# Kernel tuning notes

Measured on AMD Instinct MI355X. Metric: run time of the kernel, lower is better.

Reference implementation:

```python
import jax, jax.numpy as jnp
import numpy as np

HEADS = 12
D_MODEL = 768
D_K = D_MODEL // HEADS


def setup_inputs() -> dict:
    key = jax.random.key(0)
    ks = jax.random.split(key, 11)
    B, S, D = 2, 2048, D_MODEL
    s = 1.0 / np.sqrt(D)
    return {
        "query": jax.random.normal(ks[0], (B, S, D), jnp.float32),
        "key": jax.random.normal(ks[1], (B, S, D), jnp.float32),
        "value": jax.random.normal(ks[2], (B, S, D), jnp.float32),
        "Wq": jax.random.normal(ks[3], (D, D), jnp.float32) * s,
        "bq": jnp.zeros((D,), jnp.float32),
        "Wk": jax.random.normal(ks[4], (D, D), jnp.float32) * s,
        "bk": jnp.zeros((D,), jnp.float32),
        "Wv": jax.random.normal(ks[5], (D, D), jnp.float32) * s,
        "bv": jnp.zeros((D,), jnp.float32),
        "Wo": jax.random.normal(ks[6], (D, D), jnp.float32) * s,
        "bo": jnp.zeros((D,), jnp.float32),
    }


def reference(query, key, value, Wq, bq, Wk, bk, Wv, bv, Wo, bo):
    B, S, D = query.shape
    # linear projections (weights stored as [in, out])
    q = query @ Wq + bq
    k = key @ Wk + bk
    v = value @ Wv + bv
    # [B, H, S, d_k]
    q = q.reshape(B, S, HEADS, D_K).transpose(0, 2, 1, 3)
    k = k.reshape(B, S, HEADS, D_K).transpose(0, 2, 1, 3)
    v = v.reshape(B, S, HEADS, D_K).transpose(0, 2, 1, 3)
    # scores: note module scales by sqrt(d_k) (key.size(-1)), not self.scaled
    scores = jnp.einsum("bhqd,bhkd->bhqk", q, k) / jnp.sqrt(jnp.asarray(D_K, q.dtype))
    weights = jax.nn.softmax(scores, axis=-1)
    context = jnp.einsum("bhqk,bhkd->bhqd", weights, v)
    context = context.transpose(0, 2, 1, 3).reshape(B, S, D)
    return context @ Wo + bo
```

## Files before the change

### kernel.cpp

```cpp
#include <hip/hip_runtime.h>
#include <hip/hip_bf16.h>
#include <math.h>

#define D_MODEL 768
#define HEADS 12
#define DK 64
#define SEQ 2048
#define BATCH 2
#define MTOT (BATCH * SEQ)
#define QSCALE 0.18033688011112042f

using short8 = __attribute__((ext_vector_type(8))) short;
using us4    = __attribute__((ext_vector_type(4))) unsigned short;
using f32x4  = __attribute__((ext_vector_type(4))) float;

static __device__ __forceinline__ unsigned f2bf2(float x, float y) {
    __hip_bfloat162 t = __float22bfloat162_rn(float2{x, y});
    return *reinterpret_cast<unsigned*>(&t);
}
static __device__ __forceinline__ unsigned short f2bf1(float x) {
    __hip_bfloat16 t = __float2bfloat16(x);
    return *reinterpret_cast<unsigned short*>(&t);
}
static __device__ __forceinline__ float bf2f(unsigned short u) {
    unsigned v = (unsigned)u << 16;
    return __uint_as_float(v);
}
static __device__ __forceinline__ short8 cvt8(float4 a, float4 b) {
    union { unsigned u[4]; short8 s; } r;
    r.u[0] = f2bf2(a.x, a.y);
    r.u[1] = f2bf2(a.z, a.w);
    r.u[2] = f2bf2(b.x, b.y);
    r.u[3] = f2bf2(b.z, b.w);
    return r.s;
}
static __device__ __forceinline__ float fast_exp2(float x) {
#if __has_builtin(__builtin_amdgcn_exp2f)
    return __builtin_amdgcn_exp2f(x);
#else
    return __expf(x * 0.6931471805599453f);
#endif
}

static __device__ __forceinline__ void gload_lds16(const void* g, void* l) {
    __builtin_amdgcn_global_load_lds(
        (const __attribute__((address_space(1))) void*)g,
        (__attribute__((address_space(3))) void*)l, 16, 0, 0);
}

static __device__ __forceinline__ void barrier_lgkm() {
    asm volatile("s_waitcnt lgkmcnt(0)" ::: "memory");
    __builtin_amdgcn_s_barrier();
    __builtin_amdgcn_sched_barrier(0);
}
static __device__ __forceinline__ void barrier_vm0() {
    asm volatile("s_waitcnt vmcnt(0)" ::: "memory");
    __builtin_amdgcn_s_barrier();
    __builtin_amdgcn_sched_barrier(0);
}

__global__ __launch_bounds__(256) void cvt_wt_k(
    const float* __restrict__ Wq, const float* __restrict__ Wk,
    const float* __restrict__ Wv, const float* __restrict__ Wo,
    unsigned short* __restrict__ Wqt, unsigned short* __restrict__ Wkt,
    unsigned short* __restrict__ Wvt, unsigned short* __restrict__ Wot)
{
    const int z = blockIdx.z;
    const float* W = z == 0 ? Wq : z == 1 ? Wk : z == 2 ? Wv : Wo;
    unsigned short* Wt = z == 0 ? Wqt : z == 1 ? Wkt : z == 2 ? Wvt : Wot;
    __shared__ float t[32][33];
    const int n0 = blockIdx.x * 32, k0 = blockIdx.y * 32;
    const int tx = threadIdx.x & 31;
    const int ty0 = (threadIdx.x >> 5) * 4;
    #pragma unroll
    for (int j = 0; j < 4; ++j)
        t[ty0 + j][tx] = W[(size_t)(k0 + ty0 + j) * D_MODEL + n0 + tx];
    __syncthreads();
    #pragma unroll
    for (int j = 0; j < 4; ++j)
        Wt[(size_t)(n0 + ty0 + j) * D_MODEL + k0 + tx] = f2bf1(t[tx][ty0 + j]);
}

__global__ __launch_bounds__(512) void gemm_qkv_k(
    const float* __restrict__ query, const float* __restrict__ key,
    const float* __restrict__ value,
    const unsigned short* __restrict__ Wqt, const unsigned short* __restrict__ Wkt,
    const unsigned short* __restrict__ Wvt,
    const float* __restrict__ bq, const float* __restrict__ bk,
    const float* __restrict__ bv,
    unsigned short* __restrict__ qb, unsigned short* __restrict__ kb,
    unsigned short* __restrict__ vb)
{
    __shared__ __align__(16) char gsm[65536];

    const int bid = blockIdx.x;
    const int xcd = bid & 7;
    const int idx = bid >> 3;
    const int z   = idx / 24;
    const int rr  = idx % 24;
    const int brow = (xcd * 4 + rr / 6) * 128;
    const int bcol = (rr % 6) * 128;

    const float* A           = z == 0 ? query : z == 1 ? key : value;
    const unsigned short* Wt = z == 0 ? Wqt : z == 1 ? Wkt : Wvt;
    const float* bias        = z == 0 ? bq  : z == 1 ? bk  : bv;
    unsigned short* C        = z == 0 ? qb  : z == 1 ? kb  : vb;
    const float scale        = z == 0 ? QSCALE : 1.0f;

    const int tid  = threadIdx.x;
    const int w    = tid >> 6;
    const int lane = tid & 63;
    const int g    = lane >> 4, c = lane & 15;
    const int wr   = w >> 2, wc = w & 3;

    f32x4 acc[4][2] = {};

    const int xc  = (c & 7) << 4;
    const int rb0 = c * 128 + ((g * 16) ^ xc);
    const int rb1 = c * 128 + ((64 + g * 16) ^ xc);

    int bsrow[2], bsoff[2], bsdst[2];
    #pragma unroll
    for (int r = 0; r < 2; ++r) {
        int phys = (w * 2 + r) * 1024 + lane * 16;
        int row  = phys >> 7;
        int slot = (phys >> 4) & 7;
        bsrow[r] = row;
        bsoff[r] = (slot ^ (row & 7)) * 8;
        bsdst[r] = (w * 2 + r) * 1024;
    }
    const int ar = tid >> 2;
    const int ac = (tid & 3) << 4;
    int awa[2];
    #pragma unroll
    for (int i = 0; i < 2; ++i)
        awa[i] = ar * 128 + (((ac << 1) + 16 * i) ^ ((ar & 7) << 4));
    const float* Ap32 = A + (size_t)(brow + ar) * D_MODEL + ac;

    float4 ra0, ra1, ra2, ra3;

    auto stageB = [&](int k0, int buf) {
        #pragma unroll
        for (int r = 0; r < 2; ++r)
            gload_lds16(Wt + (size_t)(bcol + bsrow[r]) * D_MODEL + k0 + bsoff[r],
                        gsm + 32768 + buf * 16384 + bsdst[r]);
    };
    auto loadA32 = [&](int k0) {
        ra0 = *(const float4*)(Ap32 + k0);
        ra1 = *(const float4*)(Ap32 + k0 + 4);
        ra2 = *(const float4*)(Ap32 + k0 + 8);
        ra3 = *(const float4*)(Ap32 + k0 + 12);
    };
    auto writeA32 = [&](int buf) {
        *(short8*)(gsm + buf * 16384 + awa[0]) = cvt8(ra0, ra1);
        *(short8*)(gsm + buf * 16384 + awa[1]) = cvt8(ra2, ra3);
    };

    stageB(0, 0);
    loadA32(0);
    writeA32(0);
    barrier_lgkm();

    for (int k0 = 0; k0 < D_MODEL; k0 += 128) {
        #pragma unroll
        for (int u = 0; u < 2; ++u) {
            const int kn = min(k0 + u * 64 + 64, D_MODEL - 64);
            stageB(kn, u ^ 1);
            loadA32(kn);
            __builtin_amdgcn_sched_barrier(0);

            __builtin_amdgcn_s_setprio(1);
            #pragma unroll
            for (int kstep = 0; kstep < 2; ++kstep) {
                const int rb = kstep ? rb1 : rb0;
                short8 af[4], bf[2];
                #pragma unroll
                for (int m = 0; m < 4; ++m)
                    af[m] = *(const short8*)(gsm + u * 16384 + wr * 8192 +
                                             m * 2048 + rb);
                #pragma unroll
                for (int n = 0; n < 2; ++n)
                    bf[n] = *(const short8*)(gsm + 32768 + u * 16384 +
                                             wc * 4096 + n * 2048 + rb);
                #pragma unroll
                for (int m = 0; m < 4; ++m)
                    #pragma unroll
                    for (int n = 0; n < 2; ++n)
                        acc[m][n] = __builtin_amdgcn_mfma_f32_16x16x32_bf16(
                                        af[m], bf[n], acc[m][n], 0, 0, 0);
            }
            __builtin_amdgcn_s_setprio(0);

            writeA32(u ^ 1);
            barrier_lgkm();
        }
    }

    #pragma unroll
    for (int m = 0; m < 4; ++m)
        #pragma unroll
        for (int n = 0; n < 2; ++n) {
            const int col = bcol + wc * 32 + n * 16 + c;
            const float bval = bias[col];
            #pragma unroll
            for (int j = 0; j < 4; ++j) {
                const int row = brow + wr * 64 + m * 16 + g * 4 + j;
                C[(size_t)row * D_MODEL + col] = f2bf1((acc[m][n][j] + bval) * scale);
            }
        }
}

__global__ __launch_bounds__(256) void gemm_o_k(
    const unsigned short* __restrict__ A, const unsigned short* __restrict__ Wt,
    const float* __restrict__ bias, float* __restrict__ C)
{
    __shared__ __align__(16) char gsm[32768];

    const int bid = blockIdx.x;
    const int xcd = bid & 7;
    const int idx = bid >> 3;
    const int brow = (xcd * 8 + idx / 12) * 64;
    const int bcol = (idx % 12) * 64;

    const int tid  = threadIdx.x;
    const int w    = tid >> 6;
    const int lane = tid & 63;
    const int g    = lane >> 4, c = lane & 15;
    const int wr   = w >> 1, wc = w & 1;

    f32x4 acc[2][2] = {{f32x4{0,0,0,0}, f32x4{0,0,0,0}},
                       {f32x4{0,0,0,0}, f32x4{0,0,0,0}}};

    const int xc  = (c & 7) << 4;
    const int rb0 = c * 128 + ((g * 16) ^ xc);
    const int rb1 = c * 128 + ((64 + g * 16) ^ xc);
    const int a0 = rb0 + wr * 4096, a1 = rb1 + wr * 4096;
    const int b0r = rb0 + 16384 + wc * 4096, b1r = rb1 + 16384 + wc * 4096;

    int bsrow[2], bsoff[2], bsdst[2];
    #pragma unroll
    for (int r = 0; r < 2; ++r) {
        int phys = (w + 4 * r) * 1024 + lane * 16;
        int row  = phys >> 7;
        int slot = (phys >> 4) & 7;
        bsrow[r] = row;
        bsoff[r] = (slot ^ (row & 7)) * 8;
        bsdst[r] = (w + 4 * r) * 1024;
    }

    auto stage = [&](int k0, int buf) {
        #pragma unroll
        for (int r = 0; r < 2; ++r) {
            gload_lds16(A  + (size_t)(brow + bsrow[r]) * D_MODEL + k0 + bsoff[r],
                        gsm + buf * 8192 + bsdst[r]);
            gload_lds16(Wt + (size_t)(bcol + bsrow[r]) * D_MODEL + k0 + bsoff[r],
                        gsm + 16384 + buf * 8192 + bsdst[r]);
        }
    };

    stage(0, 0);
    barrier_vm0();

    for (int k0 = 0; k0 < D_MODEL; k0 += 128) {
        #pragma unroll
        for (int u = 0; u < 2; ++u) {
            const int kn = min(k0 + u * 64 + 64, D_MODEL - 64);
            stage(kn, u ^ 1);
            __builtin_amdgcn_sched_barrier(0);

            #pragma unroll
            for (int kstep = 0; kstep < 2; ++kstep) {
                short8 af[2], bf[2];
                #pragma unroll
                for (int m = 0; m < 2; ++m)
                    af[m] = *(const short8*)(gsm + u * 8192 + m * 2048 +
                                             (kstep ? a1 : a0));
                #pragma unroll
                for (int n = 0; n < 2; ++n)
                    bf[n] = *(const short8*)(gsm + u * 8192 + n * 2048 +
                                             (kstep ? b1r : b0r));
                #pragma unroll
                for (int m = 0; m < 2; ++m)
                    #pragma unroll
                    for (int n = 0; n < 2; ++n)
                        acc[m][n] = __builtin_amdgcn_mfma_f32_16x16x32_bf16(
                                        af[m], bf[n], acc[m][n], 0, 0, 0);
            }
            barrier_vm0();
        }
    }

    #pragma unroll
    for (int m = 0; m < 2; ++m)
        #pragma unroll
        for (int n = 0; n < 2; ++n) {
            const int col = bcol + wc * 32 + n * 16 + c;
            const float bval = bias[col];
            #pragma unroll
            for (int j = 0; j < 4; ++j) {
                const int row = brow + wr * 32 + m * 16 + g * 4 + j;
                C[(size_t)row * D_MODEL + col] = acc[m][n][j] + bval;
            }
        }
}

__global__ __launch_bounds__(512) void attn_mfma_k(
    const unsigned short* __restrict__ q, const unsigned short* __restrict__ k,
    const unsigned short* __restrict__ v, unsigned short* __restrict__ opart,
    float* __restrict__ mlpart)
{
    __shared__ __align__(16) char sm[49152];

    const int tid  = threadIdx.x;
    const int w    = tid >> 6;
    const int lane = tid & 63;
    const int g    = lane >> 4;
    const int c    = lane & 15;

    const int bid  = blockIdx.x;
    const int swz  = (bid & 7) * 96 + (bid >> 3);
    const int qt   = swz & 15;
    const int rest = swz >> 4;
    const int half = rest & 1;
    const int hb   = rest >> 1;
    const int h    = hb % HEADS;
    const int b    = hb / HEADS;
    const int q0   = qt * 128;
    const int NT2  = 16;

    short8 qf0, qf1;
    {
        const int qrow = q0 + (w << 4) + c;
        const unsigned short* qp = q + (size_t)(b * SEQ + qrow) * D_MODEL + h * DK;
        qf0 = *(const short8*)(qp + g * 8);
        qf1 = *(const short8*)(qp + 32 + g * 8);
    }

    float m_run[4] = {-INFINITY, -INFINITY, -INFINITY, -INFINITY};
    f32x4 lacc = f32x4{0, 0, 0, 0};
    f32x4 o[4] = {f32x4{0,0,0,0}, f32x4{0,0,0,0}, f32x4{0,0,0,0}, f32x4{0,0,0,0}};
    const short8 ONES = {0x3F80, 0x3F80, 0x3F80, 0x3F80,
                         0x3F80, 0x3F80, 0x3F80, 0x3F80};

    const int xc  = (c & 7) << 4;
    const int rb0 = c * 128 + ((g * 16) ^ xc);
    const int rb1 = c * 128 + ((64 + g * 16) ^ xc);
    const int bp0 = 32768 + w * 2048 + rb0;
    const int bp1 = 32768 + w * 2048 + rb1;

    int pwa[4];
    #pragma unroll
    for (int r = 0; r < 4; ++r) {
        const int row = (g << 2) + r;
        pwa[r] = 32768 + w * 2048 + row * 128 + ((c << 3) ^ ((row & 7) << 4));
    }
    const int cv = tid & 15, vd0 = ((tid >> 4) & 15) << 2;
    int vwa[4];
    #pragma unroll
    for (int j = 0; j < 4; ++j) {
        const int row = vd0 + j;
        vwa[j] = 16384 + row * 128 + ((cv << 3) ^ ((row & 7) << 4));
    }
    int kdst[2];
    const unsigned short* kg[2];
    {
        const unsigned short* kbase =
            k + (size_t)(b * SEQ + half * (SEQ / 2)) * D_MODEL + h * DK;
        #pragma unroll
        for (int r = 0; r < 2; ++r) {
            int phys = ((w & 3) + 4 * r) * 1024 + lane * 16;
            int row  = phys >> 7;
            int slot = (phys >> 4) & 7;
            kdst[r]  = ((w & 3) + 4 * r) * 1024;
            kg[r]    = kbase + (size_t)row * D_MODEL + (slot ^ (row & 7)) * 8;
        }
    }
    const unsigned short* vg =
        v + (size_t)(b * SEQ + half * (SEQ / 2) + cv) * D_MODEL + h * DK + vd0;
    const int TS = 64 * D_MODEL;

    us4 va, vb_, vc, vd;

    if (w < 4) {
        gload_lds16(kg[0], sm + kdst[0]);
        gload_lds16(kg[1], sm + kdst[1]);
        va  = *(const us4*)(vg);
        vb_ = *(const us4*)(vg + 16 * D_MODEL);
        vc  = *(const us4*)(vg + 32 * D_MODEL);
        vd  = *(const us4*)(vg + 48 * D_MODEL);
        #pragma unroll
        for (int j = 0; j < 4; ++j) {
            uint2 pk;
            pk.x = (unsigned)va[j] | ((unsigned)vb_[j] << 16);
            pk.y = (unsigned)vc[j] | ((unsigned)vd[j] << 16);
            *(uint2*)(sm + vwa[j]) = pk;
        }
    }
    kg[0] += TS; kg[1] += TS; vg += TS;
    barrier_lgkm();

    for (int kt = 0; kt < NT2; kt += 2) {
        #pragma unroll
        for (int u = 0; u < 2; ++u) {
            if (w < 4) {
                gload_lds16(kg[0], sm + (u ^ 1) * 8192 + kdst[0]);
                gload_lds16(kg[1], sm + (u ^ 1) * 8192 + kdst[1]);
                va  = *(const us4*)(vg);
                vb_ = *(const us4*)(vg + 16 * D_MODEL);
                vc  = *(const us4*)(vg + 32 * D_MODEL);
                vd  = *(const us4*)(vg + 48 * D_MODEL);
            }
            kg[0] += TS; kg[1] += TS; vg += TS;
            __builtin_amdgcn_sched_barrier(0);

            f32x4 sacc[4] = {f32x4{0,0,0,0}, f32x4{0,0,0,0},
                             f32x4{0,0,0,0}, f32x4{0,0,0,0}};
            __builtin_amdgcn_s_setprio(1);
            #pragma unroll
            for (int kstep = 0; kstep < 2; ++kstep) {
                short8 af = kstep ? qf1 : qf0;
                #pragma unroll
                for (int ks = 0; ks < 4; ++ks) {
                    short8 bf = *(const short8*)(sm + u * 8192 + ks * 2048 +
                                                 (kstep ? rb1 : rb0));
                    sacc[ks] = __builtin_amdgcn_mfma_f32_16x16x32_bf16(
                                   af, bf, sacc[ks], 0, 0, 0);
                }
            }
            __builtin_amdgcn_s_setprio(0);

            float rm[4], dm;
            #pragma unroll
            for (int reg = 0; reg < 4; ++reg)
                rm[reg] = fmaxf(fmaxf(sacc[0][reg], sacc[1][reg]),
                                fmaxf(sacc[2][reg], sacc[3][reg]));
            dm = fmaxf(fmaxf(rm[0] - m_run[0], rm[1] - m_run[1]),
                       fmaxf(rm[2] - m_run[2], rm[3] - m_run[3]));
            if (__any(dm > 11.0f)) {
                #pragma unroll
                for (int reg = 0; reg < 4; ++reg) {
                    float mx = rm[reg];
                    mx = fmaxf(mx, __shfl_xor(mx, 1));
                    mx = fmaxf(mx, __shfl_xor(mx, 2));
                    mx = fmaxf(mx, __shfl_xor(mx, 4));
                    mx = fmaxf(mx, __shfl_xor(mx, 8));
                    const float mnew = fmaxf(m_run[reg], mx);
                    const float sc = fast_exp2(m_run[reg] - mnew);
                    m_run[reg] = mnew;
                    lacc[reg] *= sc;
                    o[0][reg] *= sc;
                    o[1][reg] *= sc;
                    o[2][reg] *= sc;
                    o[3][reg] *= sc;
                }
            }
            #pragma unroll
            for (int reg = 0; reg < 4; ++reg) {
                const float m = m_run[reg];
                float p0 = fast_exp2(sacc[0][reg] - m);
                float p1 = fast_exp2(sacc[1][reg] - m);
                float p2 = fast_exp2(sacc[2][reg] - m);
                float p3 = fast_exp2(sacc[3][reg] - m);
                uint2 pw;
                pw.x = f2bf2(p0, p1);
                pw.y = f2bf2(p2, p3);
                *(uint2*)(sm + pwa[reg]) = pw;
            }

            __builtin_amdgcn_s_setprio(1);
            #pragma unroll
            for (int kstep = 0; kstep < 2; ++kstep) {
                short8 paf = *(const short8*)(sm + (kstep ? bp1 : bp0));
                lacc = __builtin_amdgcn_mfma_f32_16x16x32_bf16(paf, ONES, lacc, 0, 0, 0);
                #pragma unroll
                for (int dsub = 0; dsub < 4; ++dsub) {
                    short8 vbf = *(const short8*)(sm + 16384 + u * 8192 +
                                                  dsub * 2048 + (kstep ? rb1 : rb0));
                    o[dsub] = __builtin_amdgcn_mfma_f32_16x16x32_bf16(
                                  paf, vbf, o[dsub], 0, 0, 0);
                }
            }
            __builtin_amdgcn_s_setprio(0);

            if (w < 4) {
                #pragma unroll
                for (int j = 0; j < 4; ++j) {
                    uint2 pk;
                    pk.x = (unsigned)va[j] | ((unsigned)vb_[j] << 16);
                    pk.y = (unsigned)vc[j] | ((unsigned)vd[j] << 16);
                    *(uint2*)(sm + (u ^ 1) * 8192 + vwa[j]) = pk;
                }
            }
            barrier_lgkm();
        }
    }

    const size_t obase = (size_t)half * ((size_t)MTOT * D_MODEL) +
                         (size_t)(b * SEQ) * D_MODEL + h * DK;
    #pragma unroll
    for (int reg = 0; reg < 4; ++reg) {
        const int qrow = q0 + (w << 4) + (g << 2) + reg;
        unsigned short* ob = opart + obase + (size_t)qrow * D_MODEL;
        #pragma unroll
        for (int dsub = 0; dsub < 4; ++dsub)
            ob[dsub * 16 + c] = f2bf1(o[dsub][reg]);
        if (c == 0) {
            float2 mlv;
            mlv.x = m_run[reg];
            mlv.y = lacc[reg];
            ((float2*)mlpart)[(size_t)half * MTOT * HEADS +
                              (size_t)(b * SEQ + qrow) * HEADS + h] = mlv;
        }
    }
}

__global__ __launch_bounds__(256) void combine_k(
    const unsigned short* __restrict__ op, const float* __restrict__ mlpart,
    unsigned short* __restrict__ cb)
{
    const int t   = blockIdx.x * 256 + threadIdx.x;
    const int row = t / 96;
    const int gi  = t - row * 96;
    const int col = gi << 3;
    const int h   = gi >> 3;

    const float2* mlp = (const float2*)mlpart;
    const float2 ml0 = mlp[(size_t)row * HEADS + h];
    const float2 ml1 = mlp[(size_t)MTOT * HEADS + (size_t)row * HEADS + h];
    const float m  = fmaxf(ml0.x, ml1.x);
    const float s0 = fast_exp2(ml0.x - m);
    const float s1 = fast_exp2(ml1.x - m);
    const float inv = 1.0f / (ml0.y * s0 + ml1.y * s1);
    const float a0 = s0 * inv, a1 = s1 * inv;

    const size_t off = (size_t)row * D_MODEL + col;
    us4 x0  = *(const us4*)(op + off);
    us4 x0b = *(const us4*)(op + off + 4);
    us4 x1  = *(const us4*)(op + (size_t)MTOT * D_MODEL + off);
    us4 x1b = *(const us4*)(op + (size_t)MTOT * D_MODEL + off + 4);

    union { unsigned short u[8]; short8 s; } r;
    #pragma unroll
    for (int j = 0; j < 4; ++j) {
        r.u[j]     = f2bf1(bf2f(x0[j])  * a0 + bf2f(x1[j])  * a1);
        r.u[4 + j] = f2bf1(bf2f(x0b[j]) * a0 + bf2f(x1b[j]) * a1);
    }
    *(short8*)(cb + off) = r.s;
}

extern "C" void kernel_launch(void* const* d_in, const int* in_sizes, int n_in,
                              void* d_out, int out_size, void* d_ws, size_t ws_size,
                              hipStream_t stream) {
    const float* query = (const float*)d_in[0];
    const float* key   = (const float*)d_in[1];
    const float* value = (const float*)d_in[2];
    const float* Wq = (const float*)d_in[3];
    const float* bq = (const float*)d_in[4];
    const float* Wk = (const float*)d_in[5];
    const float* bk = (const float*)d_in[6];
    const float* Wv = (const float*)d_in[7];
    const float* bv = (const float*)d_in[8];
    const float* Wo = (const float*)d_in[9];
    const float* bo = (const float*)d_in[10];
    float* out = (float*)d_out;

    const size_t mat = (size_t)MTOT * D_MODEL;
    unsigned short* qb  = (unsigned short*)d_ws;
    unsigned short* kb  = qb + mat;
    unsigned short* vb  = kb + mat;
    unsigned short* cb  = vb + mat;
    unsigned short* Wqt = cb + mat;
    unsigned short* Wkt = Wqt + (size_t)D_MODEL * D_MODEL;
    unsigned short* Wvt = Wkt + (size_t)D_MODEL * D_MODEL;
    unsigned short* Wot = Wvt + (size_t)D_MODEL * D_MODEL;
    unsigned short* op  = Wot + (size_t)D_MODEL * D_MODEL;
    float*          mlp = (float*)(op + 2 * mat);

    cvt_wt_k<<<dim3(D_MODEL / 32, D_MODEL / 32, 4), 256, 0, stream>>>(
        Wq, Wk, Wv, Wo, Wqt, Wkt, Wvt, Wot);

    gemm_qkv_k<<<dim3(576), 512, 0, stream>>>(
        query, key, value, Wqt, Wkt, Wvt, bq, bk, bv, qb, kb, vb);

    attn_mfma_k<<<dim3(768), 512, 0, stream>>>(qb, kb, vb, op, mlp);

    combine_k<<<dim3(MTOT * D_MODEL / 8 / 256), 256, 0, stream>>>(op, mlp, cb);

    gemm_o_k<<<dim3(768), 256, 0, stream>>>(cb, Wot, bo, out);
}
```

Baseline: 113.4 us.

## Rewrite attention with 32x32 MFMA, register-resident P, and 4-wave blocks

The attention kernel moves from 16x16x32 to 32x32x16 bf16 MFMA. It computes S^T so that the exponentiated probabilities stay in registers and feed the PV MFMA directly, with no round trip through LDS. Blocks shrink to 4 waves of 32 query rows each, with every wave loading K/V, and LDS drops to 32KB. The V LDS layout is permuted to match the new operand layout, and m/l are split into separate arrays. This removes the P store/load and barrier traffic and may raise occupancy, at the cost of a larger accumulator register footprint and a more complex layout mapping.

```diff
diff --git a/kernel.cpp b/kernel.cpp
--- a/kernel.cpp
+++ b/kernel.cpp
@@ -13,6 +13,7 @@
 using short8 = __attribute__((ext_vector_type(8))) short;
 using us4    = __attribute__((ext_vector_type(4))) unsigned short;
 using f32x4  = __attribute__((ext_vector_type(4))) float;
+using f32x16 = __attribute__((ext_vector_type(16))) float;
 
 static __device__ __forceinline__ unsigned f2bf2(float x, float y) {
     __hip_bfloat162 t = __float22bfloat162_rn(float2{x, y});
@@ -40,6 +41,11 @@
 #else
     return __expf(x * 0.6931471805599453f);
 #endif
+}
+static __device__ __forceinline__ unsigned pk2(float lo, float hi) {
+    unsigned d;
+    asm("v_cvt_pk_bf16_f32 %0, %1, %2" : "=v"(d) : "v"(lo), "v"(hi));
+    return d;
 }
 
 static __device__ __forceinline__ void gload_lds16(const void* g, void* l) {
@@ -304,18 +310,18 @@
         }
 }
 
-__global__ __launch_bounds__(512) void attn_mfma_k(
+__global__ __launch_bounds__(256) void attn_mfma_k(
     const unsigned short* __restrict__ q, const unsigned short* __restrict__ k,
     const unsigned short* __restrict__ v, unsigned short* __restrict__ opart,
-    float* __restrict__ mlpart)
+    float* __restrict__ mpart, float* __restrict__ lpart)
 {
-    __shared__ __align__(16) char sm[49152];
+    __shared__ __align__(16) char sm[32768];
 
     const int tid  = threadIdx.x;
     const int w    = tid >> 6;
     const int lane = tid & 63;
-    const int g    = lane >> 4;
-    const int c    = lane & 15;
+    const int c    = lane & 31;
+    const int hi   = lane >> 5;
 
     const int bid  = blockIdx.x;
     const int swz  = (bid & 7) * 96 + (bid >> 3);
@@ -328,39 +334,27 @@
     const int q0   = qt * 128;
     const int NT2  = 16;
 
-    short8 qf0, qf1;
+    short8 qf[4];
     {
-        const int qrow = q0 + (w << 4) + c;
-        const unsigned short* qp = q + (size_t)(b * SEQ + qrow) * D_MODEL + h * DK;
-        qf0 = *(const short8*)(qp + g * 8);
-        qf1 = *(const short8*)(qp + 32 + g * 8);
-    }
-
-    float m_run[4] = {-INFINITY, -INFINITY, -INFINITY, -INFINITY};
-    f32x4 lacc = f32x4{0, 0, 0, 0};
-    f32x4 o[4] = {f32x4{0,0,0,0}, f32x4{0,0,0,0}, f32x4{0,0,0,0}, f32x4{0,0,0,0}};
+        const unsigned short* qp =
+            q + (size_t)(b * SEQ + q0 + w * 32 + c) * D_MODEL + h * DK;
+        #pragma unroll
+        for (int t = 0; t < 4; ++t)
+            qf[t] = *(const short8*)(qp + t * 16 + hi * 8);
+    }
+
+    float m_run = -INFINITY;
+    f32x16 lacc = {};
+    f32x16 o0 = {}, o1 = {};
     const short8 ONES = {0x3F80, 0x3F80, 0x3F80, 0x3F80,
                          0x3F80, 0x3F80, 0x3F80, 0x3F80};
 
-    const int xc  = (c & 7) << 4;
-    const int rb0 = c * 128 + ((g * 16) ^ xc);
-    const int rb1 = c * 128 + ((64 + g * 16) ^ xc);
-    const int bp0 = 32768 + w * 2048 + rb0;
-    const int bp1 = 32768 + w * 2048 + rb1;
-
-    int pwa[4];
-    #pragma unroll
-    for (int r = 0; r < 4; ++r) {
-        const int row = (g << 2) + r;
-        pwa[r] = 32768 + w * 2048 + row * 128 + ((c << 3) ^ ((row & 7) << 4));
-    }
-    const int cv = tid & 15, vd0 = ((tid >> 4) & 15) << 2;
-    int vwa[4];
-    #pragma unroll
-    for (int j = 0; j < 4; ++j) {
-        const int row = vd0 + j;
-        vwa[j] = 16384 + row * 128 + ((cv << 3) ^ ((row & 7) << 4));
-    }
+    const int xc = (c & 7) << 4;
+    int koff[4];
+    #pragma unroll
+    for (int t = 0; t < 4; ++t)
+        koff[t] = ((32 * t + 16 * hi) ^ xc) + c * 128;
+
     int kdst[2];
     const unsigned short* kg[2];
     {
@@ -368,12 +362,20 @@
             k + (size_t)(b * SEQ + half * (SEQ / 2)) * D_MODEL + h * DK;
         #pragma unroll
         for (int r = 0; r < 2; ++r) {
-            int phys = ((w & 3) + 4 * r) * 1024 + lane * 16;
+            int phys = (w + 4 * r) * 1024 + lane * 16;
             int row  = phys >> 7;
             int slot = (phys >> 4) & 7;
-            kdst[r]  = ((w & 3) + 4 * r) * 1024;
+            kdst[r]  = (w + 4 * r) * 1024;
             kg[r]    = kbase + (size_t)row * D_MODEL + (slot ^ (row & 7)) * 8;
         }
+    }
+    const int cv = tid & 15, vd0 = (tid >> 4) << 2;
+    const int vposP = 16 * (cv >> 3) + 8 * ((cv >> 2) & 1) + 2 * (cv & 3);
+    int vwa[4];
+    #pragma unroll
+    for (int j = 0; j < 4; ++j) {
+        const int row = vd0 + j;
+        vwa[j] = 16384 + row * 128 + ((2 * vposP) ^ ((row & 7) << 4));
     }
     const unsigned short* vg =
         v + (size_t)(b * SEQ + half * (SEQ / 2) + cv) * D_MODEL + h * DK + vd0;
@@ -381,116 +383,98 @@
 
     us4 va, vb_, vc, vd;
 
-    if (w < 4) {
-        gload_lds16(kg[0], sm + kdst[0]);
-        gload_lds16(kg[1], sm + kdst[1]);
+    auto issue_k = [&](int buf) {
+        gload_lds16(kg[0], sm + buf * 8192 + kdst[0]);
+        gload_lds16(kg[1], sm + buf * 8192 + kdst[1]);
+        kg[0] += TS; kg[1] += TS;
+    };
+    auto load_v = [&]() {
         va  = *(const us4*)(vg);
         vb_ = *(const us4*)(vg + 16 * D_MODEL);
         vc  = *(const us4*)(vg + 32 * D_MODEL);
         vd  = *(const us4*)(vg + 48 * D_MODEL);
+        vg += TS;
+    };
+    auto write_v = [&](int buf) {
         #pragma unroll
         for (int j = 0; j < 4; ++j) {
-            uint2 pk;
-            pk.x = (unsigned)va[j] | ((unsigned)vb_[j] << 16);
-            pk.y = (unsigned)vc[j] | ((unsigned)vd[j] << 16);
-            *(uint2*)(sm + vwa[j]) = pk;
-        }
-    }
-    kg[0] += TS; kg[1] += TS; vg += TS;
+            unsigned lo  = (unsigned)va[j]  | ((unsigned)vc[j] << 16);
+            unsigned hi2 = (unsigned)vb_[j] | ((unsigned)vd[j] << 16);
+            *(unsigned*)(sm + buf * 8192 + vwa[j])        = lo;
+            *(unsigned*)(sm + buf * 8192 + (vwa[j] ^ 64)) = hi2;
+        }
+    };
+
+    issue_k(0);
+    __builtin_amdgcn_sched_barrier(0);
+    load_v();
+    write_v(0);
     barrier_lgkm();
 
-    for (int kt = 0; kt < NT2; kt += 2) {
+    for (int kt2 = 0; kt2 < NT2; kt2 += 2) {
         #pragma unroll
         for (int u = 0; u < 2; ++u) {
-            if (w < 4) {
-                gload_lds16(kg[0], sm + (u ^ 1) * 8192 + kdst[0]);
-                gload_lds16(kg[1], sm + (u ^ 1) * 8192 + kdst[1]);
-                va  = *(const us4*)(vg);
-                vb_ = *(const us4*)(vg + 16 * D_MODEL);
-                vc  = *(const us4*)(vg + 32 * D_MODEL);
-                vd  = *(const us4*)(vg + 48 * D_MODEL);
-            }
-            kg[0] += TS; kg[1] += TS; vg += TS;
+            const int tile = kt2 + u;
+            issue_k(u ^ 1);
             __builtin_amdgcn_sched_barrier(0);
-
-            f32x4 sacc[4] = {f32x4{0,0,0,0}, f32x4{0,0,0,0},
-                             f32x4{0,0,0,0}, f32x4{0,0,0,0}};
+            load_v();
+            __builtin_amdgcn_sched_barrier(0);
+
+            f32x16 s0 = {}, s1 = {};
             __builtin_amdgcn_s_setprio(1);
             #pragma unroll
-            for (int kstep = 0; kstep < 2; ++kstep) {
-                short8 af = kstep ? qf1 : qf0;
-                #pragma unroll
-                for (int ks = 0; ks < 4; ++ks) {
-                    short8 bf = *(const short8*)(sm + u * 8192 + ks * 2048 +
-                                                 (kstep ? rb1 : rb0));
-                    sacc[ks] = __builtin_amdgcn_mfma_f32_16x16x32_bf16(
-                                   af, bf, sacc[ks], 0, 0, 0);
+            for (int t = 0; t < 4; ++t) {
+                short8 kf0 = *(const short8*)(sm + u * 8192 + koff[t]);
+                short8 kf1 = *(const short8*)(sm + u * 8192 + 4096 + koff[t]);
+                s0 = __builtin_amdgcn_mfma_f32_32x32x16_bf16(kf0, qf[t], s0, 0, 0, 0);
+                s1 = __builtin_amdgcn_mfma_f32_32x32x16_bf16(kf1, qf[t], s1, 0, 0, 0);
+            }
+            __builtin_amdgcn_s_setprio(0);
+
+            float rmax = s0[0];
+            #pragma unroll
+            for (int r = 1; r < 16; ++r) rmax = fmaxf(rmax, s0[r]);
+            #pragma unroll
+            for (int r = 0; r < 16; ++r) rmax = fmaxf(rmax, s1[r]);
+            rmax = fmaxf(rmax, __shfl_xor(rmax, 32));
+
+            if (tile == 0) {
+                m_run = rmax;
+            } else if (__any(rmax > m_run + 11.0f)) {
+                const float mnew = fmaxf(m_run, rmax);
+                const float sc = fast_exp2(m_run - mnew);
+                m_run = mnew;
+                #pragma unroll
+                for (int r = 0; r < 16; ++r) {
+                    const float scr = __shfl(sc, (r & 3) + 8 * (r >> 2) + 4 * hi);
+                    lacc[r] *= scr;
+                    o0[r] *= scr;
+                    o1[r] *= scr;
                 }
             }
+
+            #pragma unroll
+            for (int r = 0; r < 16; ++r) {
+                s0[r] = fast_exp2(s0[r] - m_run);
+                s1[r] = fast_exp2(s1[r] - m_run);
+            }
+
+            __builtin_amdgcn_s_setprio(1);
+            #pragma unroll
+            for (int t = 0; t < 4; ++t) {
+                union { unsigned u4[4]; short8 s8; } pf;
+                #pragma unroll
+                for (int j = 0; j < 4; ++j)
+                    pf.u4[j] = pk2(s0[4 * t + j], s1[4 * t + j]);
+                short8 vf0 = *(const short8*)(sm + 16384 + u * 8192 + koff[t]);
+                short8 vf1 = *(const short8*)(sm + 16384 + u * 8192 + 4096 + koff[t]);
+                lacc = __builtin_amdgcn_mfma_f32_32x32x16_bf16(pf.s8, ONES, lacc, 0, 0, 0);
+                o0 = __builtin_amdgcn_mfma_f32_32x32x16_bf16(pf.s8, vf0, o0, 0, 0, 0);
+                o1 = __builtin_amdgcn_mfma_f32_32x32x16_bf16(pf.s8, vf1, o1, 0, 0, 0);
+            }
             __builtin_amdgcn_s_setprio(0);
 
-            float rm[4], dm;
-            #pragma unroll
-            for (int reg = 0; reg < 4; ++reg)
-                rm[reg] = fmaxf(fmaxf(sacc[0][reg], sacc[1][reg]),
-                                fmaxf(sacc[2][reg], sacc[3][reg]));
-            dm = fmaxf(fmaxf(rm[0] - m_run[0], rm[1] - m_run[1]),
-                       fmaxf(rm[2] - m_run[2], rm[3] - m_run[3]));
-            if (__any(dm > 11.0f)) {
-                #pragma unroll
-                for (int reg = 0; reg < 4; ++reg) {
-                    float mx = rm[reg];
-                    mx = fmaxf(mx, __shfl_xor(mx, 1));
-                    mx = fmaxf(mx, __shfl_xor(mx, 2));
-                    mx = fmaxf(mx, __shfl_xor(mx, 4));
-                    mx = fmaxf(mx, __shfl_xor(mx, 8));
-                    const float mnew = fmaxf(m_run[reg], mx);
-                    const float sc = fast_exp2(m_run[reg] - mnew);
-                    m_run[reg] = mnew;
-                    lacc[reg] *= sc;
-                    o[0][reg] *= sc;
-                    o[1][reg] *= sc;
-                    o[2][reg] *= sc;
-                    o[3][reg] *= sc;
-                }
-            }
-            #pragma unroll
-            for (int reg = 0; reg < 4; ++reg) {
-                const float m = m_run[reg];
-                float p0 = fast_exp2(sacc[0][reg] - m);
-                float p1 = fast_exp2(sacc[1][reg] - m);
-                float p2 = fast_exp2(sacc[2][reg] - m);
-                float p3 = fast_exp2(sacc[3][reg] - m);
-                uint2 pw;
-                pw.x = f2bf2(p0, p1);
-                pw.y = f2bf2(p2, p3);
-                *(uint2*)(sm + pwa[reg]) = pw;
-            }
-
-            __builtin_amdgcn_s_setprio(1);
-            #pragma unroll
-            for (int kstep = 0; kstep < 2; ++kstep) {
-                short8 paf = *(const short8*)(sm + (kstep ? bp1 : bp0));
-                lacc = __builtin_amdgcn_mfma_f32_16x16x32_bf16(paf, ONES, lacc, 0, 0, 0);
-                #pragma unroll
-                for (int dsub = 0; dsub < 4; ++dsub) {
-                    short8 vbf = *(const short8*)(sm + 16384 + u * 8192 +
-                                                  dsub * 2048 + (kstep ? rb1 : rb0));
-                    o[dsub] = __builtin_amdgcn_mfma_f32_16x16x32_bf16(
-                                  paf, vbf, o[dsub], 0, 0, 0);
-                }
-            }
-            __builtin_amdgcn_s_setprio(0);
-
-            if (w < 4) {
-                #pragma unroll
-                for (int j = 0; j < 4; ++j) {
-                    uint2 pk;
-                    pk.x = (unsigned)va[j] | ((unsigned)vb_[j] << 16);
-                    pk.y = (unsigned)vc[j] | ((unsigned)vd[j] << 16);
-                    *(uint2*)(sm + (u ^ 1) * 8192 + vwa[j]) = pk;
-                }
-            }
+            write_v(u ^ 1);
             barrier_lgkm();
         }
     }
@@ -498,25 +482,28 @@
     const size_t obase = (size_t)half * ((size_t)MTOT * D_MODEL) +
                          (size_t)(b * SEQ) * D_MODEL + h * DK;
     #pragma unroll
-    for (int reg = 0; reg < 4; ++reg) {
-        const int qrow = q0 + (w << 4) + (g << 2) + reg;
+    for (int r = 0; r < 16; ++r) {
+        const int qrow = q0 + w * 32 + (r & 3) + 8 * (r >> 2) + 4 * hi;
         unsigned short* ob = opart + obase + (size_t)qrow * D_MODEL;
-        #pragma unroll
-        for (int dsub = 0; dsub < 4; ++dsub)
-            ob[dsub * 16 + c] = f2bf1(o[dsub][reg]);
-        if (c == 0) {
-            float2 mlv;
-            mlv.x = m_run[reg];
-            mlv.y = lacc[reg];
-            ((float2*)mlpart)[(size_t)half * MTOT * HEADS +
-                              (size_t)(b * SEQ + qrow) * HEADS + h] = mlv;
+        ob[c]      = f2bf1(o0[r]);
+        ob[32 + c] = f2bf1(o1[r]);
+    }
+    const size_t mlbase = (size_t)half * MTOT * HEADS +
+                          (size_t)(b * SEQ) * HEADS + h;
+    if (hi == 0)
+        mpart[mlbase + (size_t)(q0 + w * 32 + c) * HEADS] = m_run;
+    if (c == 0) {
+        #pragma unroll
+        for (int r = 0; r < 16; ++r) {
+            const int qrow = q0 + w * 32 + (r & 3) + 8 * (r >> 2) + 4 * hi;
+            lpart[mlbase + (size_t)qrow * HEADS] = lacc[r];
         }
     }
 }
 
 __global__ __launch_bounds__(256) void combine_k(
-    const unsigned short* __restrict__ op, const float* __restrict__ mlpart,
-    unsigned short* __restrict__ cb)
+    const unsigned short* __restrict__ op, const float* __restrict__ mp,
+    const float* __restrict__ lp, unsigned short* __restrict__ cb)
 {
     const int t   = blockIdx.x * 256 + threadIdx.x;
     const int row = t / 96;
@@ -524,13 +511,14 @@
     const int col = gi << 3;
     const int h   = gi >> 3;
 
-    const float2* mlp = (const float2*)mlpart;
-    const float2 ml0 = mlp[(size_t)row * HEADS + h];
-    const float2 ml1 = mlp[(size_t)MTOT * HEADS + (size_t)row * HEADS + h];
-    const float m  = fmaxf(ml0.x, ml1.x);
-    const float s0 = fast_exp2(ml0.x - m);
-    const float s1 = fast_exp2(ml1.x - m);
-    const float inv = 1.0f / (ml0.y * s0 + ml1.y * s1);
+    const float m0 = mp[(size_t)row * HEADS + h];
+    const float m1 = mp[(size_t)MTOT * HEADS + (size_t)row * HEADS + h];
+    const float l0 = lp[(size_t)row * HEADS + h];
+    const float l1 = lp[(size_t)MTOT * HEADS + (size_t)row * HEADS + h];
+    const float m  = fmaxf(m0, m1);
+    const float s0 = fast_exp2(m0 - m);
+    const float s1 = fast_exp2(m1 - m);
+    const float inv = 1.0f / (l0 * s0 + l1 * s1);
     const float a0 = s0 * inv, a1 = s1 * inv;
 
     const size_t off = (size_t)row * D_MODEL + col;
@@ -574,7 +562,8 @@
     unsigned short* Wvt = Wkt + (size_t)D_MODEL * D_MODEL;
     unsigned short* Wot = Wvt + (size_t)D_MODEL * D_MODEL;
     unsigned short* op  = Wot + (size_t)D_MODEL * D_MODEL;
-    float*          mlp = (float*)(op + 2 * mat);
+    float*          mp  = (float*)(op + 2 * mat);
+    float*          lp  = mp + 2 * (size_t)MTOT * HEADS;
 
     cvt_wt_k<<<dim3(D_MODEL / 32, D_MODEL / 32, 4), 256, 0, stream>>>(
         Wq, Wk, Wv, Wo, Wqt, Wkt, Wvt, Wot);
@@ -582,9 +571,9 @@
     gemm_qkv_k<<<dim3(576), 512, 0, stream>>>(
         query, key, value, Wqt, Wkt, Wvt, bq, bk, bv, qb, kb, vb);
 
-    attn_mfma_k<<<dim3(768), 512, 0, stream>>>(qb, kb, vb, op, mlp);
-
-    combine_k<<<dim3(MTOT * D_MODEL / 8 / 256), 256, 0, stream>>>(op, mlp, cb);
+    attn_mfma_k<<<dim3(768), 256, 0, stream>>>(qb, kb, vb, op, mp, lp);
+
+    combine_k<<<dim3(MTOT * D_MODEL / 8 / 256), 256, 0, stream>>>(op, mp, lp, cb);
 
     gemm_o_k<<<dim3(768), 256, 0, stream>>>(cb, Wot, bo, out);
 }
```

Result: faster. 104.8 us (-7.5%).
